# Kernel optimization log

Hardware: AMD Instinct MI355X
Metric: run time of the kernel (lower is better)

## Reference

```python
import jax, jax.numpy as jnp
import numpy as np
import math

D = 1024      # d_model
H = 4096      # expert hidden
E = 8         # num_experts
K = 2         # top_k
CAP_FACTOR = 1.25
B, S = 4, 2048
T = B * S
CAP = int(math.ceil(CAP_FACTOR * T * K / E))  # 2560


def setup_inputs() -> dict:
    key = jax.random.key(0)
    ks = jax.random.split(key, 6)
    x  = jax.random.normal(ks[0], (B, S, D), dtype=jnp.float32)
    Wr = jax.random.normal(ks[1], (D, E), dtype=jnp.float32) * (1.0 / np.sqrt(D))
    W1 = jax.random.normal(ks[2], (E, D, H), dtype=jnp.float32) * (1.0 / np.sqrt(D))
    b1 = jnp.zeros((E, H), dtype=jnp.float32)
    W2 = jax.random.normal(ks[3], (E, H, D), dtype=jnp.float32) * (1.0 / np.sqrt(H))
    b2 = jnp.zeros((E, D), dtype=jnp.float32)
    return {"x": x, "Wr": Wr, "W1": W1, "b1": b1, "W2": W2, "b2": b2}


def reference(x, Wr, W1, b1, W2, b2):
    x_flat = x.reshape(T, D)

    # ---- Router: top-k softmax gating (temp = 1.0), renormalized weights ----
    logits = jnp.einsum('td,de->te', x_flat, Wr)
    probs = jax.nn.softmax(logits, axis=-1)
    topk_w, topk_idx = jax.lax.top_k(probs, K)            # [T,K]
    topk_w = topk_w / jnp.sum(topk_w, axis=-1, keepdims=True)

    # ---- Vectorized capacity-based dispatch ----
    e = topk_idx.reshape(-1)                               # [T*K] expert id per pair
    onehot = jax.nn.one_hot(e, E, dtype=jnp.int32)         # [T*K, E]
    pos_all = jnp.cumsum(onehot, axis=0) - 1               # slot within expert
    pos = jnp.take_along_axis(pos_all, e[:, None], axis=1)[:, 0]
    keep = pos < CAP
    # dropped pairs go to a dummy slot E*CAP (sliced off / zero-padded)
    dest = jnp.where(keep, e * CAP + pos, E * CAP)         # [T*K]

    x_pairs = jnp.repeat(x_flat, K, axis=0)                # [T*K, D]
    buf = jnp.zeros((E * CAP + 1, D), dtype=x.dtype).at[dest].set(x_pairs)
    expert_in = buf[:E * CAP].reshape(E, CAP, D)

    # ---- Grouped expert MLP (GELU) ----
    h = jax.nn.gelu(jnp.einsum('ecd,edh->ech', expert_in, W1) + b1[:, None, :])
    expert_out = jnp.einsum('ech,ehd->ecd', h, W2) + b2[:, None, :]

    # ---- Combine: gather back and weight; dropped tokens get zeros ----
    out_pad = jnp.concatenate(
        [expert_out.reshape(E * CAP, D), jnp.zeros((1, D), dtype=x.dtype)], axis=0)
    y_pairs = out_pad[dest] * topk_w.reshape(-1)[:, None]  # [T*K, D]
    y_flat = y_pairs.reshape(T, K, D).sum(axis=1)
    return y_flat.reshape(B, S, D)
```

## Files before the change

### kernel.cpp

```cpp
#include <hip/hip_runtime.h>
#include <stdint.h>

#define D_MODEL 1024
#define H_DIM   4096
#define NE      8
#define NCAP    2560
#define NTOK    8192
#define NPAIR   (NTOK * 2)

typedef __attribute__((ext_vector_type(8))) __bf16 bf16x8;
typedef __attribute__((ext_vector_type(4))) float  f32x4;
typedef __attribute__((ext_vector_type(8))) unsigned short ushort8;

__device__ __forceinline__ unsigned short f2bf(float f) {
  union { float f; unsigned u; } v; v.f = f;
  unsigned r = v.u + 0x7fffu + ((v.u >> 16) & 1u);
  return (unsigned short)(r >> 16);
}
__device__ __forceinline__ float bf2f(unsigned short s) {
  union { unsigned u; float f; } v; v.u = ((unsigned)s) << 16;
  return v.f;
}
__device__ __forceinline__ float gelu_tanh(float x) {
  float u = 0.7978845608028654f * (x + 0.044715f * x * x * x);
  float e = __expf(2.0f * u);
  float th = 1.0f - 2.0f / (e + 1.0f);
  return 0.5f * x * (1.0f + th);
}
__device__ __forceinline__ void load_lds16(const void* g, void* l) {
  __builtin_amdgcn_global_load_lds(
      (const __attribute__((address_space(1))) unsigned int*)g,
      (__attribute__((address_space(3))) unsigned int*)l, 16, 0, 0);
}

__global__ __launch_bounds__(256) void router_kernel(
    const float* __restrict__ x, const float* __restrict__ Wr,
    int* __restrict__ pair_e, float* __restrict__ pair_w) {
  int lane = threadIdx.x & 63;
  int t = blockIdx.x * 4 + (threadIdx.x >> 6);
  float acc[NE];
#pragma unroll
  for (int e = 0; e < NE; ++e) acc[e] = 0.0f;
  const float* xr = x + (size_t)t * D_MODEL;
  for (int d = lane; d < D_MODEL; d += 64) {
    float xv = xr[d];
#pragma unroll
    for (int e = 0; e < NE; ++e) acc[e] = fmaf(xv, Wr[d * NE + e], acc[e]);
  }
#pragma unroll
  for (int off = 32; off > 0; off >>= 1) {
#pragma unroll
    for (int e = 0; e < NE; ++e) acc[e] += __shfl_down(acc[e], off, 64);
  }
  if (lane == 0) {
    int i1 = 0;
#pragma unroll
    for (int e = 1; e < NE; ++e) if (acc[e] > acc[i1]) i1 = e;
    int i2 = (i1 == 0) ? 1 : 0;
#pragma unroll
    for (int e = 0; e < NE; ++e) if (e != i1 && acc[e] > acc[i2]) i2 = e;
    float p2 = expf(acc[i2] - acc[i1]);
    float inv = 1.0f / (1.0f + p2);
    pair_e[t * 2]     = i1;  pair_e[t * 2 + 1] = i2;
    pair_w[t * 2]     = inv;
    pair_w[t * 2 + 1] = p2 * inv;
  }
}

__global__ __launch_bounds__(1024) void assign_kernel(
    const int* __restrict__ pair_e, int* __restrict__ pair_dest,
    int* __restrict__ counts) {
  __shared__ int wtot[16][NE];
  const int tid = threadIdx.x;
  const int lane = tid & 63, w = tid >> 6;

  int ids[16];
  const int4* pe = (const int4*)(pair_e + tid * 16);
#pragma unroll
  for (int q = 0; q < 4; ++q) {
    int4 v = pe[q];
    ids[q * 4 + 0] = v.x; ids[q * 4 + 1] = v.y;
    ids[q * 4 + 2] = v.z; ids[q * 4 + 3] = v.w;
  }
  int c[NE];
#pragma unroll
  for (int e = 0; e < NE; ++e) c[e] = 0;
#pragma unroll
  for (int j = 0; j < 16; ++j) c[ids[j]]++;

  int incl[NE];
#pragma unroll
  for (int e = 0; e < NE; ++e) incl[e] = c[e];
#pragma unroll
  for (int d = 1; d < 64; d <<= 1) {
#pragma unroll
    for (int e = 0; e < NE; ++e) {
      int u = __shfl_up(incl[e], d, 64);
      if (lane >= d) incl[e] += u;
    }
  }
  if (lane == 63) {
#pragma unroll
    for (int e = 0; e < NE; ++e) wtot[w][e] = incl[e];
  }
  __syncthreads();
  if (tid < NE) {
    int run = 0;
#pragma unroll
    for (int ww = 0; ww < 16; ++ww) {
      int t2 = wtot[ww][tid];
      wtot[ww][tid] = run;
      run += t2;
    }
    counts[tid] = run < NCAP ? run : NCAP;
  }
  __syncthreads();

  int off[NE];
#pragma unroll
  for (int e = 0; e < NE; ++e) off[e] = wtot[w][e] + incl[e] - c[e];
#pragma unroll
  for (int j = 0; j < 16; ++j) {
    int e = ids[j];
    int pos = off[e]++;
    pair_dest[tid * 16 + j] = (pos < NCAP) ? (e * NCAP + pos) : (NE * NCAP);
  }
}

__global__ __launch_bounds__(64) void dispatch_kernel(
    const float* __restrict__ x, const int* __restrict__ pair_dest,
    unsigned short* __restrict__ Xd) {
  int i = blockIdx.x;
  int dest = pair_dest[i];
  if (dest >= NE * NCAP) return;
  int lane = threadIdx.x;
  int t = i >> 1;
  const float4* xr = (const float4*)(x + (size_t)t * D_MODEL);
  ushort4* dr = (ushort4*)(Xd + (size_t)dest * D_MODEL);
#pragma unroll
  for (int c = 0; c < 4; ++c) {
    float4 v = xr[lane + c * 64];
    ushort4 o;
    o.x = f2bf(v.x); o.y = f2bf(v.y); o.z = f2bf(v.z); o.w = f2bf(v.w);
    dr[lane + c * 64] = o;
  }
}

__global__ __launch_bounds__(256) void transpose_cvt(
    const float* __restrict__ src, unsigned short* __restrict__ dst,
    int R, int C) {
  __shared__ float tile[64][65];
  int e = blockIdx.z;
  int c0 = blockIdx.x * 64, r0 = blockIdx.y * 64;
  int col = threadIdx.x & 63, rr = threadIdx.x >> 6;
  const float* s = src + (size_t)e * R * C;
#pragma unroll
  for (int it = 0; it < 16; ++it) {
    int row = it * 4 + rr;
    tile[row][col] = s[(size_t)(r0 + row) * C + c0 + col];
  }
  __syncthreads();
  unsigned short* d = dst + (size_t)e * R * C;
#pragma unroll
  for (int it = 0; it < 16; ++it) {
    int crow = it * 4 + rr;
    d[(size_t)(c0 + crow) * R + r0 + col] = f2bf(tile[col][crow]);
  }
}

__global__ __launch_bounds__(256, 4) void moe_gemm(
    const unsigned short* __restrict__ Abase,
    const unsigned short* __restrict__ Bbase,
    const float* __restrict__ bias,
    unsigned short* __restrict__ Cout,
    const int* __restrict__ counts,
    int M, int N, int K, int NBM, int do_gelu) {
  __shared__ char smem[32768];
  const int e = blockIdx.z;
  int r = blockIdx.x;
  int grp = r >> 4, lid = r & 15;
  int mg = NBM >> 2;
  int gm = grp % mg, gn = grp / mg;
  const int m0 = (gm * 4 + (lid & 3)) * 128;
  const int n0 = (gn * 4 + (lid >> 2)) * 128;
  const int cnt = counts[e];
  if (m0 >= cnt) return;

  const int tid = threadIdx.x;
  const int lane = tid & 63;
  const int wid = tid >> 6;
  const int wm = (wid & 1) * 64;
  const int wn = (wid >> 1) * 64;

  const unsigned short* A = Abase + (size_t)e * M * K;
  const unsigned short* B = Bbase + (size_t)e * N * K;

  f32x4 acc[4][4];
  f32x4 zero = {0.f, 0.f, 0.f, 0.f};
#pragma unroll
  for (int i = 0; i < 4; ++i)
#pragma unroll
    for (int j = 0; j < 4; ++j) acc[i][j] = zero;

  char* As = smem;
  char* Bs = smem + 16384;

  const unsigned short* ga[4];
  const unsigned short* gb[4];
  int ldso[4];
#pragma unroll
  for (int c = 0; c < 4; ++c) {
    int ci = c * 256 + wid * 64 + lane;
    int srow = ci >> 3;
    int sgc = (ci & 7) ^ (srow & 7);
    ga[c] = A + (size_t)(m0 + srow) * K + sgc * 8;
    gb[c] = B + (size_t)(n0 + srow) * K + sgc * 8;
    ldso[c] = (c * 256 + wid * 64) * 16;
  }

  const int KT = K >> 6;
  for (int kt = 0; kt < KT; ++kt) {
#pragma unroll
    for (int c = 0; c < 4; ++c) {
      load_lds16(ga[c], As + ldso[c]);
      ga[c] += 64;
      load_lds16(gb[c], Bs + ldso[c]);
      gb[c] += 64;
    }
    __syncthreads();
#pragma unroll
    for (int kk = 0; kk < 2; ++kk) {
      bf16x8 af[4], bfr[4];
      int lc = kk * 4 + (lane >> 4);
#pragma unroll
      for (int f = 0; f < 4; ++f) {
        int ar = wm + f * 16 + (lane & 15);
        af[f] = *(const bf16x8*)(As + ar * 128 + ((lc ^ (ar & 7)) * 16));
        int br = wn + f * 16 + (lane & 15);
        bfr[f] = *(const bf16x8*)(Bs + br * 128 + ((lc ^ (br & 7)) * 16));
      }
#pragma unroll
      for (int i = 0; i < 4; ++i)
#pragma unroll
        for (int j = 0; j < 4; ++j)
          acc[i][j] = __builtin_amdgcn_mfma_f32_16x16x32_bf16(
              af[i], bfr[j], acc[i][j], 0, 0, 0);
    }
    __syncthreads();
  }

  const float* be = bias + (size_t)e * N;
#pragma unroll
  for (int i = 0; i < 4; ++i) {
    int rbase = wm + i * 16 + (lane >> 4) * 4;
#pragma unroll
    for (int j = 0; j < 4; ++j) {
      int col = wn + j * 16 + (lane & 15);
      float bv = be[n0 + col];
#pragma unroll
      for (int r2 = 0; r2 < 4; ++r2) {
        float xv = acc[i][j][r2] + bv;
        if (do_gelu) xv = gelu_tanh(xv);
        *(unsigned short*)(smem + (rbase + r2) * 256 + col * 2) = f2bf(xv);
      }
    }
  }
  __syncthreads();
  const int r16 = tid >> 4, c16 = tid & 15;
#pragma unroll
  for (int it = 0; it < 8; ++it) {
    int row = it * 16 + r16;
    ushort8 v = *(const ushort8*)(smem + row * 256 + c16 * 16);
    *(ushort8*)(Cout + ((size_t)e * M + m0 + row) * N + n0 + c16 * 8) = v;
  }
}

__global__ __launch_bounds__(256) void combine_kernel(
    const unsigned short* __restrict__ Ebuf,
    const int* __restrict__ pair_dest,
    const float* __restrict__ pair_w,
    float* __restrict__ out) {
  int t = blockIdx.x;
  int d0 = threadIdx.x * 4;
  float4 r = {0.f, 0.f, 0.f, 0.f};
#pragma unroll
  for (int k = 0; k < 2; ++k) {
    int dest = pair_dest[t * 2 + k];
    if (dest < NE * NCAP) {
      float w = pair_w[t * 2 + k];
      ushort4 v = *(const ushort4*)(Ebuf + (size_t)dest * D_MODEL + d0);
      r.x += w * bf2f(v.x); r.y += w * bf2f(v.y);
      r.z += w * bf2f(v.z); r.w += w * bf2f(v.w);
    }
  }
  *(float4*)(out + (size_t)t * D_MODEL + d0) = r;
}

extern "C" void kernel_launch(void* const* d_in, const int* in_sizes, int n_in,
                              void* d_out, int out_size, void* d_ws, size_t ws_size,
                              hipStream_t stream) {
  const float* x  = (const float*)d_in[0];
  const float* Wr = (const float*)d_in[1];
  const float* W1 = (const float*)d_in[2];
  const float* b1 = (const float*)d_in[3];
  const float* W2 = (const float*)d_in[4];
  const float* b2 = (const float*)d_in[5];
  float* out = (float*)d_out;

  char* ws = (char*)d_ws;
  unsigned short* W1T  = (unsigned short*)(ws + 0);
  unsigned short* W2T  = (unsigned short*)(ws + 67108864);
  unsigned short* Xd   = (unsigned short*)(ws + 134217728);
  unsigned short* Ebuf = Xd;
  unsigned short* Hbuf = (unsigned short*)(ws + 176160768);
  int*   pair_e    = (int*)(ws + 343932928);
  float* pair_w    = (float*)(ws + 343998464);
  int*   pair_dest = (int*)(ws + 344064000);
  int*   counts    = (int*)(ws + 344129536);

  transpose_cvt<<<dim3(H_DIM / 64, D_MODEL / 64, NE), 256, 0, stream>>>(W1, W1T, D_MODEL, H_DIM);
  transpose_cvt<<<dim3(D_MODEL / 64, H_DIM / 64, NE), 256, 0, stream>>>(W2, W2T, H_DIM, D_MODEL);

  router_kernel<<<NTOK / 4, 256, 0, stream>>>(x, Wr, pair_e, pair_w);
  assign_kernel<<<1, 1024, 0, stream>>>(pair_e, pair_dest, counts);
  dispatch_kernel<<<NPAIR, 64, 0, stream>>>(x, pair_dest, Xd);

  moe_gemm<<<dim3((NCAP / 128) * (H_DIM / 128), 1, NE), 256, 0, stream>>>(
      Xd, W1T, b1, Hbuf, counts, NCAP, H_DIM, D_MODEL, NCAP / 128, 1);
  moe_gemm<<<dim3((NCAP / 128) * (D_MODEL / 128), 1, NE), 256, 0, stream>>>(
      Hbuf, W2T, b2, Ebuf, counts, NCAP, D_MODEL, H_DIM, NCAP / 128, 0);

  combine_kernel<<<NTOK, 256, 0, stream>>>(Ebuf, pair_dest, pair_w, out);
}
```

Measured before the change: 768.6 us.

## Vectorize weight transpose, dispatch per token, interleave experts in GEMM grid

The weight transpose-convert kernel now uses float4 loads and 16-byte bf16 stores with a repadded shared tile, replacing scalar accesses. Dispatch runs one block per token and writes both top-k copies from a single read of x, halving activation reads. The expert GEMMs switch from a 3D grid to a flat grid with the expert index in the low bits, so concurrently scheduled blocks span all experts and load-balance across CUs. The new 69-float tile stride may change LDS bank conflicts on the strided column reads.

Measured after the change: 716.7 us. 6.8% less time.

```diff
diff --git a/kernel.cpp b/kernel.cpp
--- a/kernel.cpp
+++ b/kernel.cpp
@@ -130,41 +130,51 @@
 __global__ __launch_bounds__(64) void dispatch_kernel(
     const float* __restrict__ x, const int* __restrict__ pair_dest,
     unsigned short* __restrict__ Xd) {
-  int i = blockIdx.x;
-  int dest = pair_dest[i];
-  if (dest >= NE * NCAP) return;
+  int t = blockIdx.x;
+  int d0 = pair_dest[t * 2], d1 = pair_dest[t * 2 + 1];
+  bool k0 = d0 < NE * NCAP, k1 = d1 < NE * NCAP;
+  if (!k0 && !k1) return;
   int lane = threadIdx.x;
-  int t = i >> 1;
   const float4* xr = (const float4*)(x + (size_t)t * D_MODEL);
-  ushort4* dr = (ushort4*)(Xd + (size_t)dest * D_MODEL);
+  ushort4* r0 = (ushort4*)(Xd + (size_t)d0 * D_MODEL);
+  ushort4* r1 = (ushort4*)(Xd + (size_t)d1 * D_MODEL);
 #pragma unroll
   for (int c = 0; c < 4; ++c) {
     float4 v = xr[lane + c * 64];
     ushort4 o;
     o.x = f2bf(v.x); o.y = f2bf(v.y); o.z = f2bf(v.z); o.w = f2bf(v.w);
-    dr[lane + c * 64] = o;
+    if (k0) r0[lane + c * 64] = o;
+    if (k1) r1[lane + c * 64] = o;
   }
 }
 
 __global__ __launch_bounds__(256) void transpose_cvt(
     const float* __restrict__ src, unsigned short* __restrict__ dst,
     int R, int C) {
-  __shared__ float tile[64][65];
+  __shared__ float tile[64][69];
   int e = blockIdx.z;
   int c0 = blockIdx.x * 64, r0 = blockIdx.y * 64;
-  int col = threadIdx.x & 63, rr = threadIdx.x >> 6;
-  const float* s = src + (size_t)e * R * C;
-#pragma unroll
-  for (int it = 0; it < 16; ++it) {
-    int row = it * 4 + rr;
-    tile[row][col] = s[(size_t)(r0 + row) * C + c0 + col];
+  const float* s = src + (size_t)e * R * C + (size_t)r0 * C + c0;
+  int tc = (threadIdx.x & 15) * 4;
+  int tr = threadIdx.x >> 4;
+#pragma unroll
+  for (int it = 0; it < 4; ++it) {
+    int row = tr + it * 16;
+    float4 v = *(const float4*)(s + (size_t)row * C + tc);
+    tile[row][tc]     = v.x; tile[row][tc + 1] = v.y;
+    tile[row][tc + 2] = v.z; tile[row][tc + 3] = v.w;
   }
   __syncthreads();
-  unsigned short* d = dst + (size_t)e * R * C;
-#pragma unroll
-  for (int it = 0; it < 16; ++it) {
-    int crow = it * 4 + rr;
-    d[(size_t)(c0 + crow) * R + r0 + col] = f2bf(tile[col][crow]);
+  unsigned short* d = dst + (size_t)e * R * C + (size_t)c0 * R + r0;
+  int oc  = threadIdx.x >> 3;
+  int orr = (threadIdx.x & 7) * 8;
+#pragma unroll
+  for (int it = 0; it < 2; ++it) {
+    int crow = oc + it * 32;
+    ushort8 v;
+#pragma unroll
+    for (int j = 0; j < 8; ++j) v[j] = f2bf(tile[orr + j][crow]);
+    *(ushort8*)(d + (size_t)crow * R + orr) = v;
   }
 }
 
@@ -174,10 +184,11 @@
     const float* __restrict__ bias,
     unsigned short* __restrict__ Cout,
     const int* __restrict__ counts,
-    int M, int N, int K, int NBM, int do_gelu) {
+    int M, int N, int K, int NBM, int nxpe, int do_gelu) {
   __shared__ char smem[32768];
-  const int e = blockIdx.z;
-  int r = blockIdx.x;
+  int orig = blockIdx.x;
+  const int e = orig & 7;
+  int r = orig >> 3;
   int grp = r >> 4, lid = r & 15;
   int mg = NBM >> 2;
   int gm = grp % mg, gn = grp / mg;
@@ -323,12 +334,18 @@
 
   router_kernel<<<NTOK / 4, 256, 0, stream>>>(x, Wr, pair_e, pair_w);
   assign_kernel<<<1, 1024, 0, stream>>>(pair_e, pair_dest, counts);
-  dispatch_kernel<<<NPAIR, 64, 0, stream>>>(x, pair_dest, Xd);
-
-  moe_gemm<<<dim3((NCAP / 128) * (H_DIM / 128), 1, NE), 256, 0, stream>>>(
-      Xd, W1T, b1, Hbuf, counts, NCAP, H_DIM, D_MODEL, NCAP / 128, 1);
-  moe_gemm<<<dim3((NCAP / 128) * (D_MODEL / 128), 1, NE), 256, 0, stream>>>(
-      Hbuf, W2T, b2, Ebuf, counts, NCAP, D_MODEL, H_DIM, NCAP / 128, 0);
+  dispatch_kernel<<<NTOK, 64, 0, stream>>>(x, pair_dest, Xd);
+
+  {
+    int nxpe = (NCAP / 128) * (H_DIM / 128);
+    moe_gemm<<<nxpe * NE, 256, 0, stream>>>(
+        Xd, W1T, b1, Hbuf, counts, NCAP, H_DIM, D_MODEL, NCAP / 128, nxpe, 1);
+  }
+  {
+    int nxpe = (NCAP / 128) * (D_MODEL / 128);
+    moe_gemm<<<nxpe * NE, 256, 0, stream>>>(
+        Hbuf, W2T, b2, Ebuf, counts, NCAP, D_MODEL, H_DIM, NCAP / 128, nxpe, 0);
+  }
 
   combine_kernel<<<NTOK, 256, 0, stream>>>(Ebuf, pair_dest, pair_w, out);
 }
```
